# Performance work log

Measured on AMD Instinct MI355X. Metric: run time of the kernel, lower is better.

## Reference

```python
import jax, jax.numpy as jnp
import numpy as np

NUM_GENES = 4000
NUM_PATCHES = 64
EMBED_DIM = 192
NUM_CELLS = 4096


def setup_inputs() -> dict:
    key = jax.random.key(0)
    k1, k2, k3, k4 = jax.random.split(key, 4)
    x = jax.random.normal(k1, (NUM_CELLS, NUM_GENES), dtype=jnp.float32)
    # binary gene->pathway membership mask [num_genes, num_patches]
    mask = jax.random.randint(k2, (NUM_GENES, NUM_PATCHES), 0, 2).astype(jnp.float32)
    W = jax.random.normal(k3, (NUM_GENES, NUM_PATCHES * EMBED_DIM), dtype=jnp.float32) * 0.02
    b = jax.random.normal(k4, (NUM_PATCHES * EMBED_DIM,), dtype=jnp.float32) * 0.02
    return {"x": x, "mask": mask, "W": W, "b": b}


def reference(x, mask, W, b):
    # Expand mask as in __init__: np.repeat(mask, embed_dim, axis=1)
    # -> column j belongs to pathway j // embed_dim.
    mask_rep = jnp.repeat(mask, EMBED_DIM, axis=1)  # [genes, patches*embed]
    # CustomizedLinear: dense matmul with statically masked weight.
    out = x @ (W * mask_rep) + b  # [cells, patches*embed]
    # rearrange 'h (w c) -> h c w' with c = num_patches
    out = out.reshape(NUM_CELLS, EMBED_DIM, NUM_PATCHES).transpose(0, 2, 1)
    # norm_layer=None -> Identity
    return out  # [cells, num_patches, embed_dim]
```

## Files before the change

### kernel.cpp

```cpp
#include <hip/hip_runtime.h>
#include <hip/hip_bf16.h>

#define M_CELLS 4000000 / 1000 * 1024 / 1000
#undef M_CELLS
#define M_CELLS 4096
#define N_GENES 4000
#define KP      4032
#define NKT     63
#define N_OUT   12288
#define EMB     192
#define NPATCH  64

#define BM 256
#define BN 256
#define BK 64
#define BTILE (BN * BK)

typedef __attribute__((ext_vector_type(8))) short bf16x8_t;
typedef __attribute__((ext_vector_type(8))) unsigned short u16x8_t;
typedef __attribute__((ext_vector_type(4))) float f32x4_t;

__device__ __forceinline__ unsigned short f2bf(float f) {
  __hip_bfloat16 h = __float2bfloat16(f);
  return *reinterpret_cast<unsigned short*>(&h);
}

__device__ __forceinline__ void gll16(const unsigned short* g, unsigned short* l) {
  __builtin_amdgcn_global_load_lds(
      (const __attribute__((address_space(1))) void*)g,
      (__attribute__((address_space(3))) void*)l, 16, 0, 0);
}

__global__ __launch_bounds__(256) void prepA(const float* __restrict__ x,
                                             unsigned short* __restrict__ A) {
  const int NG = M_CELLS * (KP / 8);
  for (int g = blockIdx.x * 256 + threadIdx.x; g < NG; g += 2048 * 256) {
    int row = g / (KP / 8);
    int kc  = g - row * (KP / 8);
    int k   = kc * 8;
    u16x8_t v;
    if (k < N_GENES) {
      float4 f0 = *reinterpret_cast<const float4*>(x + (size_t)row * N_GENES + k);
      float4 f1 = *reinterpret_cast<const float4*>(x + (size_t)row * N_GENES + k + 4);
      v[0] = f2bf(f0.x); v[1] = f2bf(f0.y); v[2] = f2bf(f0.z); v[3] = f2bf(f0.w);
      v[4] = f2bf(f1.x); v[5] = f2bf(f1.y); v[6] = f2bf(f1.z); v[7] = f2bf(f1.w);
    } else {
      v = (u16x8_t)0;
    }
    *reinterpret_cast<u16x8_t*>(A + (size_t)row * KP + k) = v;
  }
}

__global__ __launch_bounds__(256) void prepB2(const float* __restrict__ W,
                                              const float* __restrict__ mask,
                                              unsigned short* __restrict__ Bt) {
  __shared__ unsigned short sT[256 * 72];
  const int t  = threadIdx.x;
  const int jb = blockIdx.x;
  const int kt = blockIdx.y;
  const int j  = jb * 256 + t;
  const int pw = j / EMB;
#pragma unroll
  for (int ch = 0; ch < 8; ++ch) {
    u16x8_t v;
#pragma unroll
    for (int u = 0; u < 8; ++u) {
      int kg = kt * 64 + ch * 8 + u;
      float val = 0.f;
      if (kg < N_GENES) val = W[(size_t)kg * N_OUT + j] * mask[kg * NPATCH + pw];
      v[u] = f2bf(val);
    }
    *reinterpret_cast<u16x8_t*>(&sT[t * 72 + ch * 8]) = v;
  }
  __syncthreads();
#pragma unroll
  for (int it = 0; it < 8; ++it) {
    int f  = it * 256 + t;
    int p  = f >> 5, u = f & 31;
    int el = u >> 3, k0 = (u & 7) * 8;
    u16x8_t v = *reinterpret_cast<const u16x8_t*>(&sT[(el * 64 + p) * 72 + k0]);
    int jp0 = p * EMB + jb * 4;
    int nt  = jp0 >> 8, c = jp0 & 255;
    *reinterpret_cast<u16x8_t*>(&Bt[(size_t)(nt * NKT + kt) * BTILE + (size_t)c * 64 + u * 8]) = v;
  }
}

#define ABASE(buf, ks) (((buf) * 2 + (ks)) * 8192)
#define BBASE(buf, ks) (32768 + ((buf) * 2 + (ks)) * 8192)

__global__ __launch_bounds__(512, 2) void gemm_bf16(const unsigned short* __restrict__ A,
                                                    const unsigned short* __restrict__ Bt,
                                                    const float* __restrict__ bias,
                                                    float* __restrict__ out) {
  __shared__ unsigned short lds[65536];

  const int tid  = threadIdx.x;
  const int lane = tid & 63;
  const int wid  = tid >> 6;
  const int wm   = wid >> 2;
  const int wn   = wid & 3;
  const int lr   = lane & 15;
  const int hi   = lane >> 4;
  const int swz  = (lr >> 1) & 3;

  const int bid = blockIdx.x;
  const int xcd = bid & 7;
  const int l   = bid >> 3;
  const int mt  = l & 15;
  const int nt  = xcd * 6 + (l >> 4);
  const int m0  = mt * BM;
  const int n0  = nt * BN;

  const int aoff = (wm * 128 + lr) * 32 + ((hi ^ swz) << 3);
  const int boff = (wn * 64 + lr) * 32 + ((hi ^ swz) << 3);

  const int srow = tid >> 2;
  const int ssl  = ((tid & 3) ^ ((tid >> 3) & 3)) << 3;
  const unsigned short* aS0 = A + (size_t)(m0 + srow) * KP + ssl;
  const unsigned short* aS1 = aS0 + (size_t)128 * KP;
  const unsigned short* bS0 = Bt + (size_t)nt * NKT * BTILE + (size_t)srow * 64 + ssl;
  const unsigned short* bS1 = bS0 + 8192;

#define STAGE_A(kt, kh, buf) { \
    gll16(aS0 + (kt) * 64 + (kh) * 32, &lds[ABASE(buf, kh) + tid * 8]); \
    gll16(aS1 + (kt) * 64 + (kh) * 32, &lds[ABASE(buf, kh) + 4096 + tid * 8]); }
#define STAGE_B(kt, kh, buf) { \
    gll16(bS0 + (size_t)(kt) * BTILE + (kh) * 32, &lds[BBASE(buf, kh) + tid * 8]); \
    gll16(bS1 + (size_t)(kt) * BTILE + (kh) * 32, &lds[BBASE(buf, kh) + 4096 + tid * 8]); }

#define READ_AF(buf, ks) \
    _Pragma("unroll") for (int m_ = 0; m_ < 8; ++m_) \
      af[m_] = *reinterpret_cast<const bf16x8_t*>(&lds[ABASE(buf, ks) + aoff + m_ * 512]);
#define READ_B2(buf, ks, nh) { \
    bfr[0] = *reinterpret_cast<const bf16x8_t*>(&lds[BBASE(buf, ks) + boff + (nh) * 1024]); \
    bfr[1] = *reinterpret_cast<const bf16x8_t*>(&lds[BBASE(buf, ks) + boff + (nh) * 1024 + 512]); }

#define MFMA16(nh) \
    __builtin_amdgcn_s_setprio(1); \
    _Pragma("unroll") for (int m_ = 0; m_ < 8; ++m_) { \
      acc[m_][(nh) * 2 + 0] = __builtin_amdgcn_mfma_f32_16x16x32_bf16(af[m_], bfr[0], acc[m_][(nh) * 2 + 0], 0, 0, 0); \
      acc[m_][(nh) * 2 + 1] = __builtin_amdgcn_mfma_f32_16x16x32_bf16(af[m_], bfr[1], acc[m_][(nh) * 2 + 1], 0, 0, 0); } \
    __builtin_amdgcn_s_setprio(0);

#define PH_OPEN() \
    __builtin_amdgcn_s_barrier(); \
    asm volatile("s_waitcnt lgkmcnt(0)" ::: "memory"); \
    __builtin_amdgcn_sched_barrier(0);
#define PH_CLOSE() \
    __builtin_amdgcn_s_barrier(); \
    __builtin_amdgcn_sched_barrier(0);
#define PH_CLOSE_VM(N) \
    asm volatile("s_waitcnt vmcnt(" #N ")" ::: "memory"); \
    __builtin_amdgcn_s_barrier(); \
    __builtin_amdgcn_sched_barrier(0);

  f32x4_t acc[8][4] = {};
  bf16x8_t af[8], bfr[2];

  STAGE_A(0, 0, 0); STAGE_B(0, 0, 0);
  STAGE_A(0, 1, 0); STAGE_B(0, 1, 0);
  STAGE_A(1, 0, 1); STAGE_B(1, 0, 1);
  asm volatile("s_waitcnt vmcnt(4)" ::: "memory");
  __builtin_amdgcn_s_barrier();
  __builtin_amdgcn_sched_barrier(0);

  for (int i = 0; i < 31; ++i) {
    const int ta = 2 * i, tb = ta + 1, tc = ta + 2;
    const int td = (tb + 2 <= 62) ? tb + 2 : 62;

    READ_AF(0, 0); READ_B2(0, 0, 0);
    STAGE_A(tb, 1, 1);
    PH_OPEN(); MFMA16(0); PH_CLOSE();
    READ_B2(0, 0, 1);
    STAGE_B(tb, 1, 1);
    PH_OPEN(); MFMA16(1); PH_CLOSE_VM(8);
    READ_AF(0, 1); READ_B2(0, 1, 0);
    STAGE_A(tc, 0, 0);
    PH_OPEN(); MFMA16(0); PH_CLOSE();
    READ_B2(0, 1, 1);
    STAGE_B(tc, 0, 0);
    PH_OPEN(); MFMA16(1); PH_CLOSE_VM(8);
    READ_AF(1, 0); READ_B2(1, 0, 0);
    STAGE_A(tc, 1, 0);
    PH_OPEN(); MFMA16(0); PH_CLOSE();
    READ_B2(1, 0, 1);
    STAGE_B(tc, 1, 0);
    PH_OPEN(); MFMA16(1); PH_CLOSE_VM(8);
    READ_AF(1, 1); READ_B2(1, 1, 0);
    STAGE_A(td, 0, 1);
    PH_OPEN(); MFMA16(0); PH_CLOSE();
    READ_B2(1, 1, 1);
    STAGE_B(td, 0, 1);
    PH_OPEN(); MFMA16(1); PH_CLOSE_VM(8);
  }

  READ_AF(0, 0); READ_B2(0, 0, 0);
  PH_OPEN(); MFMA16(0); PH_CLOSE();
  READ_B2(0, 0, 1);
  PH_OPEN(); MFMA16(1); PH_CLOSE_VM(4);
  READ_AF(0, 1); READ_B2(0, 1, 0);
  PH_OPEN(); MFMA16(0); PH_CLOSE();
  READ_B2(0, 1, 1);
  PH_OPEN(); MFMA16(1);
  asm volatile("s_waitcnt vmcnt(0)" ::: "memory");
  __builtin_amdgcn_s_barrier();

#pragma unroll
  for (int n = 0; n < 4; ++n) {
    int jc = n0 + wn * 64 + n * 16 + lr;
    float bv = bias[(jc % EMB) * NPATCH + (jc / EMB)];
#pragma unroll
    for (int m = 0; m < 8; ++m) {
      int row = m0 + wm * 128 + m * 16 + hi * 4;
      float* o = out + (size_t)row * N_OUT + jc;
#pragma unroll
      for (int r = 0; r < 4; ++r)
        o[(size_t)r * N_OUT] = acc[m][n][r] + bv;
    }
  }
}

__global__ __launch_bounds__(256) void fallback_gemm(const float* __restrict__ x,
                                                     const float* __restrict__ mask,
                                                     const float* __restrict__ W,
                                                     const float* __restrict__ b,
                                                     float* __restrict__ out) {
  __shared__ float sX[64 * 33];
  __shared__ float sB2[32 * 65];
  const int t  = threadIdx.x;
  const int c0 = blockIdx.x * 64;
  const int j0 = blockIdx.y * 64;
  const int tr = t >> 4, tc = t & 15;
  float acc[4][4] = {};
  for (int k0 = 0; k0 < N_GENES; k0 += 32) {
    __syncthreads();
#pragma unroll
    for (int i = 0; i < 8; ++i) {
      int f = i * 256 + t;
      int row = f >> 5, kk = f & 31;
      sX[row * 33 + kk] = x[(size_t)(c0 + row) * N_GENES + k0 + kk];
    }
#pragma unroll
    for (int i = 0; i < 8; ++i) {
      int f = i * 256 + t;
      int kk = f >> 6, cl = f & 63;
      int jp = j0 + cl;
      int jorig = (jp % EMB) * NPATCH + jp / EMB;
      sB2[kk * 65 + cl] = W[(size_t)(k0 + kk) * N_OUT + jorig] * mask[(k0 + kk) * NPATCH + jorig / EMB];
    }
    __syncthreads();
#pragma unroll
    for (int kk = 0; kk < 32; ++kk) {
      float a[4], bb[4];
#pragma unroll
      for (int r = 0; r < 4; ++r) a[r] = sX[(tr * 4 + r) * 33 + kk];
#pragma unroll
      for (int c = 0; c < 4; ++c) bb[c] = sB2[kk * 65 + tc * 4 + c];
#pragma unroll
      for (int r = 0; r < 4; ++r)
#pragma unroll
        for (int c = 0; c < 4; ++c) acc[r][c] += a[r] * bb[c];
    }
  }
#pragma unroll
  for (int r = 0; r < 4; ++r)
#pragma unroll
    for (int c = 0; c < 4; ++c) {
      int jp = j0 + tc * 4 + c;
      int jorig = (jp % EMB) * NPATCH + jp / EMB;
      out[(size_t)(c0 + tr * 4 + r) * N_OUT + jp] = acc[r][c] + b[jorig];
    }
}

extern "C" void kernel_launch(void* const* d_in, const int* in_sizes, int n_in,
                              void* d_out, int out_size, void* d_ws, size_t ws_size,
                              hipStream_t stream) {
  const float* x    = (const float*)d_in[0];
  const float* mask = (const float*)d_in[1];
  const float* W    = (const float*)d_in[2];
  const float* b    = (const float*)d_in[3];
  float* out = (float*)d_out;

  const size_t needA = (size_t)M_CELLS * KP * sizeof(unsigned short);
  const size_t needB = (size_t)N_OUT * KP * sizeof(unsigned short);

  if (ws_size >= needA + needB) {
    unsigned short* Abf = (unsigned short*)d_ws;
    unsigned short* Bt  = (unsigned short*)((char*)d_ws + needA);
    prepA<<<2048, 256, 0, stream>>>(x, Abf);
    prepB2<<<dim3(48, 63), 256, 0, stream>>>(W, mask, Bt);
    gemm_bf16<<<768, 512, 0, stream>>>(Abf, Bt, b, out);
  } else {
    fallback_gemm<<<dim3(64, 192), 256, 0, stream>>>(x, mask, W, b, out);
  }
}
```

Baseline: 489.5 us.

## Double-buffer GEMM register fragments and merge prep kernels into one launch

The GEMM main loop now double-buffers the A and B fragment registers, so LDS reads for the next phase are issued before the current MFMA block runs. Fine-grained lgkmcnt waits replace the full drain, and each phase uses one barrier instead of two. Separately, the two prep kernels (x to bf16, masked W to transposed bf16 tiles) are merged into a single launch to save a launch and the gap between them. This costs more registers, which could cause spills at 2 waves per SIMD, and the altered barrier and wait placement needs care to avoid LDS read/write hazards.

```diff
diff --git a/kernel.cpp b/kernel.cpp
--- a/kernel.cpp
+++ b/kernel.cpp
@@ -1,8 +1,6 @@
 #include <hip/hip_runtime.h>
 #include <hip/hip_bf16.h>
 
-#define M_CELLS 4000000 / 1000 * 1024 / 1000
-#undef M_CELLS
 #define M_CELLS 4096
 #define N_GENES 4000
 #define KP      4032
@@ -31,57 +29,59 @@
       (__attribute__((address_space(3))) void*)l, 16, 0, 0);
 }
 
-__global__ __launch_bounds__(256) void prepA(const float* __restrict__ x,
-                                             unsigned short* __restrict__ A) {
-  const int NG = M_CELLS * (KP / 8);
-  for (int g = blockIdx.x * 256 + threadIdx.x; g < NG; g += 2048 * 256) {
-    int row = g / (KP / 8);
-    int kc  = g - row * (KP / 8);
-    int k   = kc * 8;
-    u16x8_t v;
-    if (k < N_GENES) {
-      float4 f0 = *reinterpret_cast<const float4*>(x + (size_t)row * N_GENES + k);
-      float4 f1 = *reinterpret_cast<const float4*>(x + (size_t)row * N_GENES + k + 4);
-      v[0] = f2bf(f0.x); v[1] = f2bf(f0.y); v[2] = f2bf(f0.z); v[3] = f2bf(f0.w);
-      v[4] = f2bf(f1.x); v[5] = f2bf(f1.y); v[6] = f2bf(f1.z); v[7] = f2bf(f1.w);
-    } else {
-      v = (u16x8_t)0;
-    }
-    *reinterpret_cast<u16x8_t*>(A + (size_t)row * KP + k) = v;
-  }
-}
-
-__global__ __launch_bounds__(256) void prepB2(const float* __restrict__ W,
-                                              const float* __restrict__ mask,
-                                              unsigned short* __restrict__ Bt) {
+__global__ __launch_bounds__(256) void prep_fused(const float* __restrict__ x,
+                                                  const float* __restrict__ mask,
+                                                  const float* __restrict__ W,
+                                                  unsigned short* __restrict__ A,
+                                                  unsigned short* __restrict__ Bt) {
   __shared__ unsigned short sT[256 * 72];
-  const int t  = threadIdx.x;
-  const int jb = blockIdx.x;
-  const int kt = blockIdx.y;
-  const int j  = jb * 256 + t;
-  const int pw = j / EMB;
-#pragma unroll
-  for (int ch = 0; ch < 8; ++ch) {
-    u16x8_t v;
-#pragma unroll
-    for (int u = 0; u < 8; ++u) {
-      int kg = kt * 64 + ch * 8 + u;
-      float val = 0.f;
-      if (kg < N_GENES) val = W[(size_t)kg * N_OUT + j] * mask[kg * NPATCH + pw];
-      v[u] = f2bf(val);
-    }
-    *reinterpret_cast<u16x8_t*>(&sT[t * 72 + ch * 8]) = v;
-  }
-  __syncthreads();
-#pragma unroll
-  for (int it = 0; it < 8; ++it) {
-    int f  = it * 256 + t;
-    int p  = f >> 5, u = f & 31;
-    int el = u >> 3, k0 = (u & 7) * 8;
-    u16x8_t v = *reinterpret_cast<const u16x8_t*>(&sT[(el * 64 + p) * 72 + k0]);
-    int jp0 = p * EMB + jb * 4;
-    int nt  = jp0 >> 8, c = jp0 & 255;
-    *reinterpret_cast<u16x8_t*>(&Bt[(size_t)(nt * NKT + kt) * BTILE + (size_t)c * 64 + u * 8]) = v;
+  const int t = threadIdx.x;
+  if (blockIdx.x < 1024) {
+    const int NG = M_CELLS * (KP / 8);
+    for (int g = blockIdx.x * 256 + t; g < NG; g += 1024 * 256) {
+      int row = g / (KP / 8);
+      int kc  = g - row * (KP / 8);
+      int k   = kc * 8;
+      u16x8_t v;
+      if (k < N_GENES) {
+        float4 f0 = *reinterpret_cast<const float4*>(x + (size_t)row * N_GENES + k);
+        float4 f1 = *reinterpret_cast<const float4*>(x + (size_t)row * N_GENES + k + 4);
+        v[0] = f2bf(f0.x); v[1] = f2bf(f0.y); v[2] = f2bf(f0.z); v[3] = f2bf(f0.w);
+        v[4] = f2bf(f1.x); v[5] = f2bf(f1.y); v[6] = f2bf(f1.z); v[7] = f2bf(f1.w);
+      } else {
+        v = (u16x8_t)0;
+      }
+      *reinterpret_cast<u16x8_t*>(A + (size_t)row * KP + k) = v;
+    }
+  } else {
+    const int idx = blockIdx.x - 1024;
+    const int jb  = idx % 48;
+    const int kt  = idx / 48;
+    const int j   = jb * 256 + t;
+    const int pw  = j / EMB;
+#pragma unroll
+    for (int ch = 0; ch < 8; ++ch) {
+      u16x8_t v;
+#pragma unroll
+      for (int u = 0; u < 8; ++u) {
+        int kg = kt * 64 + ch * 8 + u;
+        float val = 0.f;
+        if (kg < N_GENES) val = W[(size_t)kg * N_OUT + j] * mask[kg * NPATCH + pw];
+        v[u] = f2bf(val);
+      }
+      *reinterpret_cast<u16x8_t*>(&sT[t * 72 + ch * 8]) = v;
+    }
+    __syncthreads();
+#pragma unroll
+    for (int it = 0; it < 8; ++it) {
+      int f  = it * 256 + t;
+      int p  = f >> 5, u = f & 31;
+      int el = u >> 3, k0 = (u & 7) * 8;
+      u16x8_t v = *reinterpret_cast<const u16x8_t*>(&sT[(el * 64 + p) * 72 + k0]);
+      int jp0 = p * EMB + jb * 4;
+      int nt  = jp0 >> 8, c = jp0 & 255;
+      *reinterpret_cast<u16x8_t*>(&Bt[(size_t)(nt * NKT + kt) * BTILE + (size_t)c * 64 + u * 8]) = v;
+    }
   }
 }
 
@@ -128,82 +128,84 @@
     gll16(bS0 + (size_t)(kt) * BTILE + (kh) * 32, &lds[BBASE(buf, kh) + tid * 8]); \
     gll16(bS1 + (size_t)(kt) * BTILE + (kh) * 32, &lds[BBASE(buf, kh) + 4096 + tid * 8]); }
 
-#define READ_AF(buf, ks) \
+#define RD_AF(bk, buf, ks) \
     _Pragma("unroll") for (int m_ = 0; m_ < 8; ++m_) \
-      af[m_] = *reinterpret_cast<const bf16x8_t*>(&lds[ABASE(buf, ks) + aoff + m_ * 512]);
-#define READ_B2(buf, ks, nh) { \
-    bfr[0] = *reinterpret_cast<const bf16x8_t*>(&lds[BBASE(buf, ks) + boff + (nh) * 1024]); \
-    bfr[1] = *reinterpret_cast<const bf16x8_t*>(&lds[BBASE(buf, ks) + boff + (nh) * 1024 + 512]); }
-
-#define MFMA16(nh) \
+      af[bk][m_] = *reinterpret_cast<const bf16x8_t*>(&lds[ABASE(buf, ks) + aoff + m_ * 512]);
+#define RD_B(bk, buf, ks, nh) { \
+    bfr[bk][0] = *reinterpret_cast<const bf16x8_t*>(&lds[BBASE(buf, ks) + boff + (nh) * 1024]); \
+    bfr[bk][1] = *reinterpret_cast<const bf16x8_t*>(&lds[BBASE(buf, ks) + boff + (nh) * 1024 + 512]); }
+
+#define MM(abk, bbk, nh) \
     __builtin_amdgcn_s_setprio(1); \
     _Pragma("unroll") for (int m_ = 0; m_ < 8; ++m_) { \
-      acc[m_][(nh) * 2 + 0] = __builtin_amdgcn_mfma_f32_16x16x32_bf16(af[m_], bfr[0], acc[m_][(nh) * 2 + 0], 0, 0, 0); \
-      acc[m_][(nh) * 2 + 1] = __builtin_amdgcn_mfma_f32_16x16x32_bf16(af[m_], bfr[1], acc[m_][(nh) * 2 + 1], 0, 0, 0); } \
+      acc[m_][(nh)*2+0] = __builtin_amdgcn_mfma_f32_16x16x32_bf16(af[abk][m_], bfr[bbk][0], acc[m_][(nh)*2+0], 0, 0, 0); \
+      acc[m_][(nh)*2+1] = __builtin_amdgcn_mfma_f32_16x16x32_bf16(af[abk][m_], bfr[bbk][1], acc[m_][(nh)*2+1], 0, 0, 0); } \
     __builtin_amdgcn_s_setprio(0);
 
-#define PH_OPEN() \
-    __builtin_amdgcn_s_barrier(); \
-    asm volatile("s_waitcnt lgkmcnt(0)" ::: "memory"); \
+#define LGKM(n) asm volatile("s_waitcnt lgkmcnt(" #n ")" ::: "memory"); \
     __builtin_amdgcn_sched_barrier(0);
-#define PH_CLOSE() \
-    __builtin_amdgcn_s_barrier(); \
-    __builtin_amdgcn_sched_barrier(0);
-#define PH_CLOSE_VM(N) \
-    asm volatile("s_waitcnt vmcnt(" #N ")" ::: "memory"); \
-    __builtin_amdgcn_s_barrier(); \
-    __builtin_amdgcn_sched_barrier(0);
+#define VMC(n)  asm volatile("s_waitcnt vmcnt(" #n ")" ::: "memory");
+#define BARC()  __builtin_amdgcn_s_barrier(); __builtin_amdgcn_sched_barrier(0);
 
   f32x4_t acc[8][4] = {};
-  bf16x8_t af[8], bfr[2];
+  bf16x8_t af[2][8], bfr[2][2];
 
   STAGE_A(0, 0, 0); STAGE_B(0, 0, 0);
   STAGE_A(0, 1, 0); STAGE_B(0, 1, 0);
   STAGE_A(1, 0, 1); STAGE_B(1, 0, 1);
-  asm volatile("s_waitcnt vmcnt(4)" ::: "memory");
-  __builtin_amdgcn_s_barrier();
-  __builtin_amdgcn_sched_barrier(0);
+  VMC(8);
+  BARC();
+  RD_AF(0, 0, 0); RD_B(0, 0, 0, 0);
 
   for (int i = 0; i < 31; ++i) {
-    const int ta = 2 * i, tb = ta + 1, tc = ta + 2;
+    const int tb = 2 * i + 1, tc = 2 * i + 2;
     const int td = (tb + 2 <= 62) ? tb + 2 : 62;
 
-    READ_AF(0, 0); READ_B2(0, 0, 0);
+    RD_B(1, 0, 0, 1);
     STAGE_A(tb, 1, 1);
-    PH_OPEN(); MFMA16(0); PH_CLOSE();
-    READ_B2(0, 0, 1);
+    LGKM(2); MM(0, 0, 0);
+    VMC(6); BARC();
+    RD_AF(1, 0, 1); RD_B(0, 0, 1, 0);
     STAGE_B(tb, 1, 1);
-    PH_OPEN(); MFMA16(1); PH_CLOSE_VM(8);
-    READ_AF(0, 1); READ_B2(0, 1, 0);
+    LGKM(10); MM(0, 1, 1);
+    BARC();
+    RD_B(1, 0, 1, 1);
     STAGE_A(tc, 0, 0);
-    PH_OPEN(); MFMA16(0); PH_CLOSE();
-    READ_B2(0, 1, 1);
+    LGKM(2); MM(1, 0, 0);
+    VMC(6); BARC();
+    RD_AF(0, 1, 0); RD_B(0, 1, 0, 0);
     STAGE_B(tc, 0, 0);
-    PH_OPEN(); MFMA16(1); PH_CLOSE_VM(8);
-    READ_AF(1, 0); READ_B2(1, 0, 0);
+    LGKM(10); MM(1, 1, 1);
+    BARC();
+    RD_B(1, 1, 0, 1);
     STAGE_A(tc, 1, 0);
-    PH_OPEN(); MFMA16(0); PH_CLOSE();
-    READ_B2(1, 0, 1);
+    LGKM(2); MM(0, 0, 0);
+    VMC(6); BARC();
+    RD_AF(1, 1, 1); RD_B(0, 1, 1, 0);
     STAGE_B(tc, 1, 0);
-    PH_OPEN(); MFMA16(1); PH_CLOSE_VM(8);
-    READ_AF(1, 1); READ_B2(1, 1, 0);
+    LGKM(10); MM(0, 1, 1);
+    BARC();
+    RD_B(1, 1, 1, 1);
     STAGE_A(td, 0, 1);
-    PH_OPEN(); MFMA16(0); PH_CLOSE();
-    READ_B2(1, 1, 1);
+    LGKM(2); MM(1, 0, 0);
+    VMC(6); BARC();
+    RD_AF(0, 0, 0); RD_B(0, 0, 0, 0);
     STAGE_B(td, 0, 1);
-    PH_OPEN(); MFMA16(1); PH_CLOSE_VM(8);
-  }
-
-  READ_AF(0, 0); READ_B2(0, 0, 0);
-  PH_OPEN(); MFMA16(0); PH_CLOSE();
-  READ_B2(0, 0, 1);
-  PH_OPEN(); MFMA16(1); PH_CLOSE_VM(4);
-  READ_AF(0, 1); READ_B2(0, 1, 0);
-  PH_OPEN(); MFMA16(0); PH_CLOSE();
-  READ_B2(0, 1, 1);
-  PH_OPEN(); MFMA16(1);
-  asm volatile("s_waitcnt vmcnt(0)" ::: "memory");
-  __builtin_amdgcn_s_barrier();
+    LGKM(10); MM(1, 1, 1);
+    BARC();
+  }
+
+  RD_B(1, 0, 0, 1);
+  LGKM(2); MM(0, 0, 0);
+  VMC(4); BARC();
+  RD_AF(1, 0, 1); RD_B(0, 0, 1, 0);
+  LGKM(10); MM(0, 1, 1);
+  BARC();
+  RD_B(1, 0, 1, 1);
+  LGKM(2); MM(1, 0, 0);
+  BARC();
+  LGKM(0); MM(1, 1, 1);
+  VMC(0);
 
 #pragma unroll
   for (int n = 0; n < 4; ++n) {
@@ -287,8 +289,7 @@
   if (ws_size >= needA + needB) {
     unsigned short* Abf = (unsigned short*)d_ws;
     unsigned short* Bt  = (unsigned short*)((char*)d_ws + needA);
-    prepA<<<2048, 256, 0, stream>>>(x, Abf);
-    prepB2<<<dim3(48, 63), 256, 0, stream>>>(W, mask, Bt);
+    prep_fused<<<4048, 256, 0, stream>>>(x, mask, W, Abf, Bt);
     gemm_bf16<<<768, 512, 0, stream>>>(Abf, Bt, b, out);
   } else {
     fallback_gemm<<<dim3(64, 192), 256, 0, stream>>>(x, mask, W, b, out);
```

Result: slower. 686.6 us (+40.3%).

## Fuse input prep kernels and reorder GEMM fragment loads by M-half

Applied to the files above, without the earlier changes.

Merges the two conversion kernels (x to bf16, masked W to tiled bf16) into a single launch whose blocks are split by index, removing one launch and letting both prep jobs run concurrently. The GEMM inner phase is restructured to load 4 A fragments and 4 B fragments per phase and compute a 4x4 MFMA block per half of M, instead of 8 A and 2 B. This changes the register footprint and the LDS read pattern, and moves the global-load wait points. The risk is that the new vmcnt(6) placement hurts latency hiding or adds LDS pressure.

```diff
diff --git a/kernel.cpp b/kernel.cpp
--- a/kernel.cpp
+++ b/kernel.cpp
@@ -1,8 +1,6 @@
 #include <hip/hip_runtime.h>
 #include <hip/hip_bf16.h>
 
-#define M_CELLS 4000000 / 1000 * 1024 / 1000
-#undef M_CELLS
 #define M_CELLS 4096
 #define N_GENES 4000
 #define KP      4032
@@ -31,57 +29,59 @@
       (__attribute__((address_space(3))) void*)l, 16, 0, 0);
 }
 
-__global__ __launch_bounds__(256) void prepA(const float* __restrict__ x,
-                                             unsigned short* __restrict__ A) {
-  const int NG = M_CELLS * (KP / 8);
-  for (int g = blockIdx.x * 256 + threadIdx.x; g < NG; g += 2048 * 256) {
-    int row = g / (KP / 8);
-    int kc  = g - row * (KP / 8);
-    int k   = kc * 8;
-    u16x8_t v;
-    if (k < N_GENES) {
-      float4 f0 = *reinterpret_cast<const float4*>(x + (size_t)row * N_GENES + k);
-      float4 f1 = *reinterpret_cast<const float4*>(x + (size_t)row * N_GENES + k + 4);
-      v[0] = f2bf(f0.x); v[1] = f2bf(f0.y); v[2] = f2bf(f0.z); v[3] = f2bf(f0.w);
-      v[4] = f2bf(f1.x); v[5] = f2bf(f1.y); v[6] = f2bf(f1.z); v[7] = f2bf(f1.w);
-    } else {
-      v = (u16x8_t)0;
-    }
-    *reinterpret_cast<u16x8_t*>(A + (size_t)row * KP + k) = v;
-  }
-}
-
-__global__ __launch_bounds__(256) void prepB2(const float* __restrict__ W,
-                                              const float* __restrict__ mask,
-                                              unsigned short* __restrict__ Bt) {
+__global__ __launch_bounds__(256) void prep_fused(const float* __restrict__ x,
+                                                  const float* __restrict__ mask,
+                                                  const float* __restrict__ W,
+                                                  unsigned short* __restrict__ A,
+                                                  unsigned short* __restrict__ Bt) {
   __shared__ unsigned short sT[256 * 72];
-  const int t  = threadIdx.x;
-  const int jb = blockIdx.x;
-  const int kt = blockIdx.y;
-  const int j  = jb * 256 + t;
-  const int pw = j / EMB;
-#pragma unroll
-  for (int ch = 0; ch < 8; ++ch) {
-    u16x8_t v;
-#pragma unroll
-    for (int u = 0; u < 8; ++u) {
-      int kg = kt * 64 + ch * 8 + u;
-      float val = 0.f;
-      if (kg < N_GENES) val = W[(size_t)kg * N_OUT + j] * mask[kg * NPATCH + pw];
-      v[u] = f2bf(val);
-    }
-    *reinterpret_cast<u16x8_t*>(&sT[t * 72 + ch * 8]) = v;
-  }
-  __syncthreads();
-#pragma unroll
-  for (int it = 0; it < 8; ++it) {
-    int f  = it * 256 + t;
-    int p  = f >> 5, u = f & 31;
-    int el = u >> 3, k0 = (u & 7) * 8;
-    u16x8_t v = *reinterpret_cast<const u16x8_t*>(&sT[(el * 64 + p) * 72 + k0]);
-    int jp0 = p * EMB + jb * 4;
-    int nt  = jp0 >> 8, c = jp0 & 255;
-    *reinterpret_cast<u16x8_t*>(&Bt[(size_t)(nt * NKT + kt) * BTILE + (size_t)c * 64 + u * 8]) = v;
+  const int t = threadIdx.x;
+  if (blockIdx.x < 1024) {
+    const int NG = M_CELLS * (KP / 8);
+    for (int g = blockIdx.x * 256 + t; g < NG; g += 1024 * 256) {
+      int row = g / (KP / 8);
+      int kc  = g - row * (KP / 8);
+      int k   = kc * 8;
+      u16x8_t v;
+      if (k < N_GENES) {
+        float4 f0 = *reinterpret_cast<const float4*>(x + (size_t)row * N_GENES + k);
+        float4 f1 = *reinterpret_cast<const float4*>(x + (size_t)row * N_GENES + k + 4);
+        v[0] = f2bf(f0.x); v[1] = f2bf(f0.y); v[2] = f2bf(f0.z); v[3] = f2bf(f0.w);
+        v[4] = f2bf(f1.x); v[5] = f2bf(f1.y); v[6] = f2bf(f1.z); v[7] = f2bf(f1.w);
+      } else {
+        v = (u16x8_t)0;
+      }
+      *reinterpret_cast<u16x8_t*>(A + (size_t)row * KP + k) = v;
+    }
+  } else {
+    const int idx = blockIdx.x - 1024;
+    const int jb  = idx % 48;
+    const int kt  = idx / 48;
+    const int j   = jb * 256 + t;
+    const int pw  = j / EMB;
+#pragma unroll
+    for (int ch = 0; ch < 8; ++ch) {
+      u16x8_t v;
+#pragma unroll
+      for (int u = 0; u < 8; ++u) {
+        int kg = kt * 64 + ch * 8 + u;
+        float val = 0.f;
+        if (kg < N_GENES) val = W[(size_t)kg * N_OUT + j] * mask[kg * NPATCH + pw];
+        v[u] = f2bf(val);
+      }
+      *reinterpret_cast<u16x8_t*>(&sT[t * 72 + ch * 8]) = v;
+    }
+    __syncthreads();
+#pragma unroll
+    for (int it = 0; it < 8; ++it) {
+      int f  = it * 256 + t;
+      int p  = f >> 5, u = f & 31;
+      int el = u >> 3, k0 = (u & 7) * 8;
+      u16x8_t v = *reinterpret_cast<const u16x8_t*>(&sT[(el * 64 + p) * 72 + k0]);
+      int jp0 = p * EMB + jb * 4;
+      int nt  = jp0 >> 8, c = jp0 & 255;
+      *reinterpret_cast<u16x8_t*>(&Bt[(size_t)(nt * NKT + kt) * BTILE + (size_t)c * 64 + u * 8]) = v;
+    }
   }
 }
 
@@ -128,18 +128,19 @@
     gll16(bS0 + (size_t)(kt) * BTILE + (kh) * 32, &lds[BBASE(buf, kh) + tid * 8]); \
     gll16(bS1 + (size_t)(kt) * BTILE + (kh) * 32, &lds[BBASE(buf, kh) + 4096 + tid * 8]); }
 
-#define READ_AF(buf, ks) \
-    _Pragma("unroll") for (int m_ = 0; m_ < 8; ++m_) \
-      af[m_] = *reinterpret_cast<const bf16x8_t*>(&lds[ABASE(buf, ks) + aoff + m_ * 512]);
-#define READ_B2(buf, ks, nh) { \
-    bfr[0] = *reinterpret_cast<const bf16x8_t*>(&lds[BBASE(buf, ks) + boff + (nh) * 1024]); \
-    bfr[1] = *reinterpret_cast<const bf16x8_t*>(&lds[BBASE(buf, ks) + boff + (nh) * 1024 + 512]); }
-
-#define MFMA16(nh) \
+#define RD_A4(buf, ks, mh) \
+    _Pragma("unroll") for (int m_ = 0; m_ < 4; ++m_) \
+      af[m_] = *reinterpret_cast<const bf16x8_t*>(&lds[ABASE(buf, ks) + aoff + ((mh) * 4 + m_) * 512]);
+#define RD_B4(buf, ks) \
+    _Pragma("unroll") for (int n_ = 0; n_ < 4; ++n_) \
+      bfr[n_] = *reinterpret_cast<const bf16x8_t*>(&lds[BBASE(buf, ks) + boff + n_ * 512]);
+
+#define MM16(mh) \
     __builtin_amdgcn_s_setprio(1); \
-    _Pragma("unroll") for (int m_ = 0; m_ < 8; ++m_) { \
-      acc[m_][(nh) * 2 + 0] = __builtin_amdgcn_mfma_f32_16x16x32_bf16(af[m_], bfr[0], acc[m_][(nh) * 2 + 0], 0, 0, 0); \
-      acc[m_][(nh) * 2 + 1] = __builtin_amdgcn_mfma_f32_16x16x32_bf16(af[m_], bfr[1], acc[m_][(nh) * 2 + 1], 0, 0, 0); } \
+    _Pragma("unroll") for (int m_ = 0; m_ < 4; ++m_) \
+    _Pragma("unroll") for (int n_ = 0; n_ < 4; ++n_) \
+      acc[(mh) * 4 + m_][n_] = __builtin_amdgcn_mfma_f32_16x16x32_bf16( \
+          af[m_], bfr[n_], acc[(mh) * 4 + m_][n_], 0, 0, 0); \
     __builtin_amdgcn_s_setprio(0);
 
 #define PH_OPEN() \
@@ -155,7 +156,7 @@
     __builtin_amdgcn_sched_barrier(0);
 
   f32x4_t acc[8][4] = {};
-  bf16x8_t af[8], bfr[2];
+  bf16x8_t af[4], bfr[4];
 
   STAGE_A(0, 0, 0); STAGE_B(0, 0, 0);
   STAGE_A(0, 1, 0); STAGE_B(0, 1, 0);
@@ -165,43 +166,43 @@
   __builtin_amdgcn_sched_barrier(0);
 
   for (int i = 0; i < 31; ++i) {
-    const int ta = 2 * i, tb = ta + 1, tc = ta + 2;
+    const int tb = 2 * i + 1, tc = 2 * i + 2;
     const int td = (tb + 2 <= 62) ? tb + 2 : 62;
 
-    READ_AF(0, 0); READ_B2(0, 0, 0);
+    RD_A4(0, 0, 0); RD_B4(0, 0);
     STAGE_A(tb, 1, 1);
-    PH_OPEN(); MFMA16(0); PH_CLOSE();
-    READ_B2(0, 0, 1);
+    PH_OPEN(); MM16(0); PH_CLOSE_VM(6);
+    RD_A4(0, 0, 1);
     STAGE_B(tb, 1, 1);
-    PH_OPEN(); MFMA16(1); PH_CLOSE_VM(8);
-    READ_AF(0, 1); READ_B2(0, 1, 0);
+    PH_OPEN(); MM16(1); PH_CLOSE();
+    RD_A4(0, 1, 0); RD_B4(0, 1);
     STAGE_A(tc, 0, 0);
-    PH_OPEN(); MFMA16(0); PH_CLOSE();
-    READ_B2(0, 1, 1);
+    PH_OPEN(); MM16(0); PH_CLOSE_VM(6);
+    RD_A4(0, 1, 1);
     STAGE_B(tc, 0, 0);
-    PH_OPEN(); MFMA16(1); PH_CLOSE_VM(8);
-    READ_AF(1, 0); READ_B2(1, 0, 0);
+    PH_OPEN(); MM16(1); PH_CLOSE();
+    RD_A4(1, 0, 0); RD_B4(1, 0);
     STAGE_A(tc, 1, 0);
-    PH_OPEN(); MFMA16(0); PH_CLOSE();
-    READ_B2(1, 0, 1);
+    PH_OPEN(); MM16(0); PH_CLOSE_VM(6);
+    RD_A4(1, 0, 1);
     STAGE_B(tc, 1, 0);
-    PH_OPEN(); MFMA16(1); PH_CLOSE_VM(8);
-    READ_AF(1, 1); READ_B2(1, 1, 0);
+    PH_OPEN(); MM16(1); PH_CLOSE();
+    RD_A4(1, 1, 0); RD_B4(1, 1);
     STAGE_A(td, 0, 1);
-    PH_OPEN(); MFMA16(0); PH_CLOSE();
-    READ_B2(1, 1, 1);
+    PH_OPEN(); MM16(0); PH_CLOSE_VM(6);
+    RD_A4(1, 1, 1);
     STAGE_B(td, 0, 1);
-    PH_OPEN(); MFMA16(1); PH_CLOSE_VM(8);
-  }
-
-  READ_AF(0, 0); READ_B2(0, 0, 0);
-  PH_OPEN(); MFMA16(0); PH_CLOSE();
-  READ_B2(0, 0, 1);
-  PH_OPEN(); MFMA16(1); PH_CLOSE_VM(4);
-  READ_AF(0, 1); READ_B2(0, 1, 0);
-  PH_OPEN(); MFMA16(0); PH_CLOSE();
-  READ_B2(0, 1, 1);
-  PH_OPEN(); MFMA16(1);
+    PH_OPEN(); MM16(1); PH_CLOSE();
+  }
+
+  RD_A4(0, 0, 0); RD_B4(0, 0);
+  PH_OPEN(); MM16(0); PH_CLOSE_VM(4);
+  RD_A4(0, 0, 1);
+  PH_OPEN(); MM16(1); PH_CLOSE();
+  RD_A4(0, 1, 0); RD_B4(0, 1);
+  PH_OPEN(); MM16(0); PH_CLOSE();
+  RD_A4(0, 1, 1);
+  PH_OPEN(); MM16(1);
   asm volatile("s_waitcnt vmcnt(0)" ::: "memory");
   __builtin_amdgcn_s_barrier();
 
@@ -287,8 +288,7 @@
   if (ws_size >= needA + needB) {
     unsigned short* Abf = (unsigned short*)d_ws;
     unsigned short* Bt  = (unsigned short*)((char*)d_ws + needA);
-    prepA<<<2048, 256, 0, stream>>>(x, Abf);
-    prepB2<<<dim3(48, 63), 256, 0, stream>>>(W, mask, Bt);
+    prep_fused<<<4048, 256, 0, stream>>>(x, mask, W, Abf, Bt);
     gemm_bf16<<<768, 512, 0, stream>>>(Abf, Bt, b, out);
   } else {
     fallback_gemm<<<dim3(64, 192), 256, 0, stream>>>(x, mask, W, b, out);
```

Measured after the change: 487.6 us. About the same (-0.4%).
